# Performance work log

Measured on AMD Instinct MI355X. Metric: run time of the kernel, lower is better.

The kernel has to match this reference:

```python
import jax, jax.numpy as jnp
import numpy as np

B, T, H, NH = 2, 2048, 2048, 16
HD = H // NH
EPS = 1e-5

def gelu_tanh(x):
    c = jnp.sqrt(jnp.asarray(2.0 / jnp.pi, x.dtype))
    return 0.5 * x * (1.0 + jnp.tanh(c * (x + 0.044715 * x * x * x)))

def layer_norm(x, scale, shift):
    mean = jnp.mean(x, axis=-1, keepdims=True)
    var = jnp.mean((x - mean) ** 2, axis=-1, keepdims=True)  # unbiased=False
    return scale * ((x - mean) / jnp.sqrt(var + EPS)) + shift

def setup_inputs() -> dict:
    key = jax.random.key(0)
    ks = jax.random.split(key, 8)
    s = 0.02
    return {
        "x": jax.random.normal(ks[0], (B, T, H), dtype=jnp.float32),
        "wq": jax.random.normal(ks[1], (H, H), dtype=jnp.float32) * s,
        "wk": jax.random.normal(ks[2], (H, H), dtype=jnp.float32) * s,
        "wv": jax.random.normal(ks[3], (H, H), dtype=jnp.float32) * s,
        "wo": jax.random.normal(ks[4], (H, H), dtype=jnp.float32) * s,
        "ln1_scale": jnp.ones((H,), jnp.float32),
        "ln1_shift": jnp.zeros((H,), jnp.float32),
        "ln2_scale": jnp.ones((H,), jnp.float32),
        "ln2_shift": jnp.zeros((H,), jnp.float32),
        "w1": jax.random.normal(ks[5], (H, 4 * H), dtype=jnp.float32) * s,
        "b1": jnp.zeros((4 * H,), jnp.float32),
        "w2": jax.random.normal(ks[6], (4 * H, H), dtype=jnp.float32) * s,
        "b2": jnp.zeros((H,), jnp.float32),
    }

def reference(x, wq, wk, wv, wo, ln1_scale, ln1_shift, ln2_scale, ln2_shift, w1, b1, w2, b2):
    b, t, c = x.shape
    # --- attention sublayer (pre-norm, residual) ---
    h = layer_norm(x, ln1_scale, ln1_shift)
    q = (h @ wq).reshape(b, t, NH, HD).transpose(0, 2, 1, 3)  # [b,nh,t,hd]
    k = (h @ wk).reshape(b, t, NH, HD).transpose(0, 2, 1, 3)
    v = (h @ wv).reshape(b, t, NH, HD).transpose(0, 2, 1, 3)
    scores = jnp.einsum('bhqd,bhkd->bhqk', q, k) / jnp.sqrt(jnp.asarray(HD, jnp.float32))
    causal = jnp.triu(jnp.ones((t, t), jnp.bool_), k=1)
    scores = jnp.where(causal, -jnp.inf, scores)
    weights = jax.nn.softmax(scores, axis=-1)
    attn = jnp.einsum('bhqk,bhkd->bhqd', weights, v)
    attn = attn.transpose(0, 2, 1, 3).reshape(b, t, c)
    x = x + attn @ wo  # dropout is identity (drop_rate=0)
    # --- FFN sublayer ---
    h = layer_norm(x, ln2_scale, ln2_shift)
    h = gelu_tanh(h @ w1 + b1) @ w2 + b2
    return x + h
```

## Files before the change

kernel.cpp:

```cpp
#include <hip/hip_runtime.h>
#include <math.h>

#define HDIM 2048
#define NTOK 4096
#define NHEAD 16
#define HEADD 128
#define TSEQ 2048
#define NBATCH 2

typedef float f32x4 __attribute__((ext_vector_type(4)));
typedef short bf16x8 __attribute__((ext_vector_type(8)));

__device__ __forceinline__ unsigned short f2bf(float f) {
  union { float f; unsigned u; } v; v.f = f;
  unsigned r = v.u + 0x7FFFu + ((v.u >> 16) & 1u);
  return (unsigned short)(r >> 16);
}

__device__ __forceinline__ float gelu_tanh_f(float x) {
  float z = 0.7978845608028654f * (x + 0.044715f * x * x * x);
  float e = __expf(2.f * z);
  float th = 1.f - 2.f / (e + 1.f);
  return 0.5f * x * (1.f + th);
}

#define GLL16(g, l) __builtin_amdgcn_global_load_lds( \
    (const __attribute__((address_space(1))) unsigned int*)(g), \
    (__attribute__((address_space(3))) unsigned int*)(l), 16, 0, 0)

__global__ __launch_bounds__(256) void ln_kernel(const float* __restrict__ in,
                                                 const float* __restrict__ scale,
                                                 const float* __restrict__ shift,
                                                 unsigned short* __restrict__ out) {
  int row = blockIdx.x;
  int t = threadIdx.x;
  const float4* r4 = (const float4*)(in + (size_t)row * HDIM);
  float4 v0 = r4[t];
  float4 v1 = r4[t + 256];
  float sum = v0.x + v0.y + v0.z + v0.w + v1.x + v1.y + v1.z + v1.w;
  float sq  = v0.x*v0.x + v0.y*v0.y + v0.z*v0.z + v0.w*v0.w +
              v1.x*v1.x + v1.y*v1.y + v1.z*v1.z + v1.w*v1.w;
  for (int o = 32; o > 0; o >>= 1) {
    sum += __shfl_down(sum, o);
    sq  += __shfl_down(sq, o);
  }
  __shared__ float red[8];
  __shared__ float stat[2];
  int lane = t & 63, w = t >> 6;
  if (lane == 0) { red[w] = sum; red[4 + w] = sq; }
  __syncthreads();
  if (t == 0) {
    float s = red[0] + red[1] + red[2] + red[3];
    float q = red[4] + red[5] + red[6] + red[7];
    float mean = s / HDIM;
    float var = q / HDIM - mean * mean;
    stat[0] = mean;
    stat[1] = rsqrtf(var + 1e-5f);
  }
  __syncthreads();
  float mean = stat[0], rstd = stat[1];
  const float4* sc4 = (const float4*)scale;
  const float4* sh4 = (const float4*)shift;
  float4 s0 = sc4[t], s1 = sc4[t + 256];
  float4 h0 = sh4[t], h1 = sh4[t + 256];
  ushort4 a, b;
  a.x = f2bf(s0.x * ((v0.x - mean) * rstd) + h0.x);
  a.y = f2bf(s0.y * ((v0.y - mean) * rstd) + h0.y);
  a.z = f2bf(s0.z * ((v0.z - mean) * rstd) + h0.z);
  a.w = f2bf(s0.w * ((v0.w - mean) * rstd) + h0.w);
  b.x = f2bf(s1.x * ((v1.x - mean) * rstd) + h1.x);
  b.y = f2bf(s1.y * ((v1.y - mean) * rstd) + h1.y);
  b.z = f2bf(s1.z * ((v1.z - mean) * rstd) + h1.z);
  b.w = f2bf(s1.w * ((v1.w - mean) * rstd) + h1.w);
  *(ushort4*)&out[(size_t)row * HDIM + t * 4] = a;
  *(ushort4*)&out[(size_t)row * HDIM + 1024 + t * 4] = b;
}

__global__ __launch_bounds__(256) void castT_kernel(const float* __restrict__ W,
                                                    unsigned short* __restrict__ Wt,
                                                    int K, int N) {
  __shared__ float T[64][65];
  int k0 = blockIdx.x * 64, n0 = blockIdx.y * 64;
  int c = threadIdx.x & 15, r = threadIdx.x >> 4;
#pragma unroll
  for (int p = 0; p < 4; p++) {
    int kr = r + p * 16;
    float4 v = *(const float4*)&W[(size_t)(k0 + kr) * N + n0 + c * 4];
    T[kr][c * 4 + 0] = v.x; T[kr][c * 4 + 1] = v.y;
    T[kr][c * 4 + 2] = v.z; T[kr][c * 4 + 3] = v.w;
  }
  __syncthreads();
#pragma unroll
  for (int p = 0; p < 4; p++) {
    int nr = r + p * 16;
    ushort4 o;
    o.x = f2bf(T[c * 4 + 0][nr]);
    o.y = f2bf(T[c * 4 + 1][nr]);
    o.z = f2bf(T[c * 4 + 2][nr]);
    o.w = f2bf(T[c * 4 + 3][nr]);
    *(ushort4*)&Wt[(size_t)(n0 + nr) * K + k0 + c * 4] = o;
  }
}

template<int BN>
__global__ __launch_bounds__(512, 2) void gemm256(const unsigned short* __restrict__ A,
                                                  const unsigned short* __restrict__ Bt,
                                                  float* __restrict__ Cf,
                                                  unsigned short* __restrict__ Cb,
                                                  const float* __restrict__ bias,
                                                  const float* __restrict__ resid,
                                                  int M, int N, int K, int act_gelu,
                                                  int qkv_mode,
                                                  unsigned short* __restrict__ Qo,
                                                  unsigned short* __restrict__ Ko,
                                                  unsigned short* __restrict__ Vto,
                                                  int rm, int rn, int xc) {
  constexpr int NIT = BN / 64;
  constexpr int NB  = NIT / 2;
  constexpr int BSZ = BN * 64;

  __shared__ unsigned short ldsA[2 * 16384];
  __shared__ unsigned short ldsB[2 * BSZ];

  const int tid = threadIdx.x;
  const int w = tid >> 6, lane = tid & 63;
  const int lm = lane & 15, qd = lane >> 4;
  const int wm = w >> 2, wn = w & 3;
  const int l8 = lane >> 3, l7 = lane & 7;

  int flat = blockIdx.y * gridDim.x + blockIdx.x;
  int xcd = flat & 7, l = flat >> 3;
  int tn_l = l % rn, tm_l = l / rn;
  int tm = (xcd / xc) * rm + tm_l;
  int tn = (xcd % xc) * rn + tn_l;
  int m0 = tm * 256, n0 = tn * BN;

  const int swz = ((l7 ^ (l8 & 7)) << 3);
  const int arb = wm * 128 + (w & 3) * 16;
  const unsigned short* pAs = A + (size_t)(m0 + arb + l8) * K + swz;
  unsigned short* lAs = ldsA + arb * 64;
  const int brb = (BN == 256) ? ((w >> 1) * 64 + (w & 1) * 16)
                              : ((w >> 1) * 32 + (w & 1) * 8);
  const unsigned short* pBs = Bt + (size_t)(n0 + brb + l8) * K + swz;
  unsigned short* lBs = ldsB + brb * 64;

  const int ca0 = ((qd ^ l7) << 3);
  const unsigned short* pAr = ldsA + (wm * 128 + lm) * 64;
  const unsigned short* pBr = ldsB + (wn * (BN / 4) + lm) * 64;

  f32x4 acc[8][NIT] = {};
  bf16x8 a[2][4], b[2][NB];

#define STAGE_A(buf, qm, kt) do { \
    const unsigned short* _s = pAs + (size_t)(qm) * 64 * K + (size_t)(kt) * 64; \
    unsigned short* _d = lAs + (buf) * 16384 + (qm) * 4096; \
    GLL16(_s, _d); \
    GLL16(_s + (size_t)8 * K, _d + 512); \
  } while (0)

#define STAGE_B(buf, qn, kt) do { \
    if (BN == 256) { \
      const unsigned short* _s = pBs + (size_t)(qn) * 32 * K + (size_t)(kt) * 64; \
      unsigned short* _d = lBs + (buf) * BSZ + (qn) * 2048; \
      GLL16(_s, _d); \
      GLL16(_s + (size_t)8 * K, _d + 512); \
    } else { \
      const unsigned short* _s = pBs + (size_t)(qn) * 16 * K + (size_t)(kt) * 64; \
      unsigned short* _d = lBs + (buf) * BSZ + (qn) * 1024; \
      GLL16(_s, _d); \
    } \
  } while (0)

#define LDA(buf, qm) do { \
    _Pragma("unroll") \
    for (int mi = 0; mi < 4; mi++) { \
      a[0][mi] = *(const bf16x8*)(pAr + (buf) * 16384 + (qm) * 4096 + mi * 1024 + ca0); \
      a[1][mi] = *(const bf16x8*)(pAr + (buf) * 16384 + (qm) * 4096 + mi * 1024 + (ca0 ^ 32)); \
    } \
  } while (0)

#define LDB(buf, qn) do { \
    _Pragma("unroll") \
    for (int ni = 0; ni < NB; ni++) { \
      b[0][ni] = *(const bf16x8*)(pBr + (buf) * BSZ + (qn) * (NB * 1024) + ni * 1024 + ca0); \
      b[1][ni] = *(const bf16x8*)(pBr + (buf) * BSZ + (qn) * (NB * 1024) + ni * 1024 + (ca0 ^ 32)); \
    } \
  } while (0)

#define MFMA_PH(qm, qn) do { \
    __builtin_amdgcn_s_setprio(1); \
    _Pragma("unroll") \
    for (int ks = 0; ks < 2; ks++) \
      _Pragma("unroll") \
      for (int mi = 0; mi < 4; mi++) \
        _Pragma("unroll") \
        for (int ni = 0; ni < NB; ni++) \
          acc[(qm) * 4 + mi][(qn) * NB + ni] = __builtin_amdgcn_mfma_f32_16x16x32_bf16( \
              a[ks][mi], b[ks][ni], acc[(qm) * 4 + mi][(qn) * NB + ni], 0, 0, 0); \
    __builtin_amdgcn_s_setprio(0); \
  } while (0)

#define BARX() do { __builtin_amdgcn_sched_barrier(0); __builtin_amdgcn_s_barrier(); \
                    __builtin_amdgcn_sched_barrier(0); } while (0)
#define LGKM0() do { asm volatile("s_waitcnt lgkmcnt(0)"); \
                     __builtin_amdgcn_sched_barrier(0); } while (0)
#define VM_SS() do { if (BN == 256) asm volatile("s_waitcnt vmcnt(6)"); \
                     else           asm volatile("s_waitcnt vmcnt(5)"); \
                     __builtin_amdgcn_sched_barrier(0); } while (0)
#define VM_0()  do { asm volatile("s_waitcnt vmcnt(0)"); \
                     __builtin_amdgcn_sched_barrier(0); } while (0)

  const int niter = K >> 7;

  STAGE_A(0, 0, 0); STAGE_B(0, 1, 0); STAGE_A(0, 1, 0); STAGE_B(0, 0, 0);
  STAGE_A(1, 0, 1); STAGE_B(1, 1, 1); STAGE_A(1, 1, 1);
  VM_SS();
  BARX();

  for (int i = 0; i < niter; ++i) {
    const bool pf = (i + 1 < niter);
    const int te = 2 * i + 2, to = 2 * i + 3;
    LDA(0, 0); LDB(0, 0);
    STAGE_B(1, 0, 2 * i + 1);
    BARX(); LGKM0();
    MFMA_PH(0, 0);
    BARX();
    LDB(0, 1);
    if (pf) STAGE_A(0, 0, te);
    BARX(); LGKM0();
    MFMA_PH(0, 1);
    BARX();
    LDA(0, 1);
    if (pf) STAGE_B(0, 1, te);
    BARX(); LGKM0();
    MFMA_PH(1, 1);
    BARX();
    LDB(0, 0);
    if (pf) STAGE_A(0, 1, te);
    BARX(); LGKM0();
    MFMA_PH(1, 0);
    if (pf) VM_SS(); else VM_0();
    BARX();
    LDA(1, 0); LDB(1, 0);
    if (pf) STAGE_B(0, 0, te);
    BARX(); LGKM0();
    MFMA_PH(0, 0);
    BARX();
    LDB(1, 1);
    if (pf) STAGE_A(1, 0, to);
    BARX(); LGKM0();
    MFMA_PH(0, 1);
    BARX();
    LDA(1, 1);
    if (pf) STAGE_B(1, 1, to);
    BARX(); LGKM0();
    MFMA_PH(1, 1);
    BARX();
    LDB(1, 0);
    if (pf) STAGE_A(1, 1, to);
    BARX(); LGKM0();
    MFMA_PH(1, 0);
    if (pf) VM_SS();
    BARX();
  }

#undef STAGE_A
#undef STAGE_B
#undef LDA
#undef LDB
#undef MFMA_PH
#undef BARX
#undef LGKM0
#undef VM_SS
#undef VM_0

  if (qkv_mode) {
#pragma unroll
    for (int ni = 0; ni < NIT; ni++) {
      int n = n0 + wn * (BN / 4) + ni * 16 + lm;
      int region = n >> 11;
      int h = (n & 2047) >> 7, d = n & 127;
#pragma unroll
      for (int mi = 0; mi < 8; mi++) {
        int mb = m0 + wm * 128 + mi * 16 + qd * 4;
        int bb = mb >> 11, t0 = mb & 2047;
        if (region == 2) {
          ushort4 u;
          u.x = f2bf(acc[mi][ni][0]); u.y = f2bf(acc[mi][ni][1]);
          u.z = f2bf(acc[mi][ni][2]); u.w = f2bf(acc[mi][ni][3]);
          *(ushort4*)&Vto[(((size_t)(bb * NHEAD + h)) * HEADD + d) * TSEQ + t0] = u;
        } else {
          unsigned short* dst = (region == 0) ? Qo : Ko;
          size_t base2 = (((size_t)(bb * NHEAD + h)) * TSEQ + t0) * HEADD + d;
#pragma unroll
          for (int r = 0; r < 4; r++)
            dst[base2 + (size_t)r * HEADD] = f2bf(acc[mi][ni][r]);
        }
      }
    }
    return;
  }

#pragma unroll
  for (int ni = 0; ni < NIT; ni++) {
    int n = n0 + wn * (BN / 4) + ni * 16 + lm;
    float bv = bias ? bias[n] : 0.f;
#pragma unroll
    for (int mi = 0; mi < 8; mi++) {
#pragma unroll
      for (int r = 0; r < 4; r++) {
        int m = m0 + wm * 128 + mi * 16 + qd * 4 + r;
        float v = acc[mi][ni][r] + bv;
        if (act_gelu) v = gelu_tanh_f(v);
        if (resid) v += resid[(size_t)m * N + n];
        if (Cb) Cb[(size_t)m * N + n] = f2bf(v);
        else Cf[(size_t)m * N + n] = v;
      }
    }
  }
}

__global__ __launch_bounds__(256, 4) void attn_mfma(const unsigned short* __restrict__ Qb,
                                                    const unsigned short* __restrict__ Kb,
                                                    const unsigned short* __restrict__ Vtb,
                                                    unsigned short* __restrict__ O) {
  __shared__ unsigned short ldsK[64 * 128];
  __shared__ unsigned short ldsV[128 * 64];
  __shared__ unsigned short ldsP[64 * 64];

  int tid = threadIdx.x;
  int w = tid >> 6, lane = tid & 63;
  int lm = lane & 15, qd = lane >> 4;
  int qt = blockIdx.x, hh = blockIdx.y, bb = blockIdx.z;
  int q0 = qt * 64;
  size_t hbase = (size_t)(bb * NHEAD + hh) * (size_t)(TSEQ * HEADD);
  const unsigned short* Qh = Qb + hbase;
  const unsigned short* Kh = Kb + hbase;
  const unsigned short* Vh = Vtb + hbase;

  bf16x8 qf[4];
  {
    const unsigned short* qp = Qh + (size_t)(q0 + w * 16 + lm) * HEADD + qd * 8;
#pragma unroll
    for (int kc = 0; kc < 4; kc++) qf[kc] = *(const bf16x8*)(qp + kc * 32);
  }

  int koff[4], voff[4], ldst[4];
#pragma unroll
  for (int it = 0; it < 4; it++) {
    int ci = it * 256 + w * 64 + lane;
    int key = ci >> 4, pos = ci & 15;
    koff[it] = key * HEADD + ((pos ^ (key & 15)) << 3);
    int d = ci >> 3, pv = ci & 7;
    voff[it] = d * TSEQ + ((pv ^ (d & 7)) << 3);
    ldst[it] = (it * 256 + w * 64) * 8;
  }

  f32x4 oacc[8] = {};
  float mrow[4], lrow[4];
#pragma unroll
  for (int r = 0; r < 4; r++) { mrow[r] = -3.0e38f; lrow[r] = 0.f; }
  const float scl = 0.08838834764831845f;

  for (int kt = 0; kt <= qt; kt++) {
    int k0 = kt * 64;
    __syncthreads();
#pragma unroll
    for (int it = 0; it < 4; it++) {
      GLL16(Kh + (size_t)k0 * HEADD + koff[it], ldsK + ldst[it]);
      GLL16(Vh + k0 + voff[it], ldsV + ldst[it]);
    }
    __syncthreads();

    f32x4 sacc[4] = {};
#pragma unroll
    for (int kb = 0; kb < 4; kb++) {
#pragma unroll
      for (int kc = 0; kc < 4; kc++) {
        bf16x8 kf = *(const bf16x8*)(ldsK + (kb * 16 + lm) * HEADD + (((kc * 4 + qd) ^ lm) << 3));
        sacc[kb] = __builtin_amdgcn_mfma_f32_16x16x32_bf16(qf[kc], kf, sacc[kb], 0, 0, 0);
      }
    }

    float sv[4][4];
    int qrow_g = q0 + w * 16 + qd * 4;
    bool diag = (kt == qt);
#pragma unroll
    for (int kb = 0; kb < 4; kb++) {
      int key_g = k0 + kb * 16 + lm;
#pragma unroll
      for (int r = 0; r < 4; r++) {
        float x = sacc[kb][r] * scl;
        sv[kb][r] = (diag && key_g > qrow_g + r) ? -3.0e38f : x;
      }
    }
    float mloc[4];
#pragma unroll
    for (int r = 0; r < 4; r++)
      mloc[r] = fmaxf(fmaxf(sv[0][r], sv[1][r]), fmaxf(sv[2][r], sv[3][r]));
#pragma unroll
    for (int dm = 1; dm < 16; dm <<= 1)
#pragma unroll
      for (int r = 0; r < 4; r++) mloc[r] = fmaxf(mloc[r], __shfl_xor(mloc[r], dm));
    float al[4], lloc[4];
#pragma unroll
    for (int r = 0; r < 4; r++) {
      float mnew = fmaxf(mrow[r], mloc[r]);
      al[r] = __expf(mrow[r] - mnew);
      mrow[r] = mnew;
      lloc[r] = 0.f;
    }
#pragma unroll
    for (int kb = 0; kb < 4; kb++) {
#pragma unroll
      for (int r = 0; r < 4; r++) {
        float p = __expf(sv[kb][r] - mrow[r]);
        lloc[r] += p;
        int row = w * 16 + qd * 4 + r;
        int chunk = (kb * 2 + (lm >> 3)) ^ (row & 7);
        ldsP[row * 64 + chunk * 8 + (lm & 7)] = f2bf(p);
      }
    }
#pragma unroll
    for (int dm = 1; dm < 16; dm <<= 1)
#pragma unroll
      for (int r = 0; r < 4; r++) lloc[r] += __shfl_xor(lloc[r], dm);
#pragma unroll
    for (int r = 0; r < 4; r++) lrow[r] = lrow[r] * al[r] + lloc[r];
#pragma unroll
    for (int dt = 0; dt < 8; dt++)
#pragma unroll
      for (int r = 0; r < 4; r++) oacc[dt][r] *= al[r];

    bf16x8 pf[2];
#pragma unroll
    for (int kc2 = 0; kc2 < 2; kc2++)
      pf[kc2] = *(const bf16x8*)(ldsP + (w * 16 + lm) * 64 + (((kc2 * 4 + qd) ^ (lm & 7)) << 3));
#pragma unroll
    for (int dt = 0; dt < 8; dt++) {
#pragma unroll
      for (int kc2 = 0; kc2 < 2; kc2++) {
        bf16x8 vf = *(const bf16x8*)(ldsV + (dt * 16 + lm) * 64 + (((kc2 * 4 + qd) ^ (lm & 7)) << 3));
        oacc[dt] = __builtin_amdgcn_mfma_f32_16x16x32_bf16(pf[kc2], vf, oacc[dt], 0, 0, 0);
      }
    }
  }

  float inv[4];
#pragma unroll
  for (int r = 0; r < 4; r++) inv[r] = 1.f / lrow[r];
#pragma unroll
  for (int dt = 0; dt < 8; dt++) {
#pragma unroll
    for (int r = 0; r < 4; r++) {
      int t = q0 + w * 16 + qd * 4 + r;
      size_t idx = ((size_t)(bb * TSEQ + t)) * HDIM + hh * HEADD + dt * 16 + lm;
      O[idx] = f2bf(oacc[dt][r] * inv[r]);
    }
  }
}

extern "C" void kernel_launch(void* const* d_in, const int* in_sizes, int n_in,
                              void* d_out, int out_size, void* d_ws, size_t ws_size,
                              hipStream_t stream) {
  const float* x         = (const float*)d_in[0];
  const float* wq        = (const float*)d_in[1];
  const float* wk        = (const float*)d_in[2];
  const float* wv        = (const float*)d_in[3];
  const float* wo        = (const float*)d_in[4];
  const float* ln1_scale = (const float*)d_in[5];
  const float* ln1_shift = (const float*)d_in[6];
  const float* ln2_scale = (const float*)d_in[7];
  const float* ln2_shift = (const float*)d_in[8];
  const float* w1        = (const float*)d_in[9];
  const float* b1        = (const float*)d_in[10];
  const float* w2        = (const float*)d_in[11];
  const float* b2        = (const float*)d_in[12];

  char* ws = (char*)d_ws;
  const size_t MB = 1ull << 20;
  unsigned short* h1    = (unsigned short*)(ws);
  float*          x2    = (float*)(ws);
  unsigned short* Qb    = (unsigned short*)(ws + 32 * MB);
  unsigned short* Kb    = (unsigned short*)(ws + 48 * MB);
  unsigned short* Vtb   = (unsigned short*)(ws + 64 * MB);
  unsigned short* attnO = (unsigned short*)(ws + 80 * MB);
  unsigned short* woT   = (unsigned short*)(ws + 96 * MB);
  unsigned short* qkvT  = (unsigned short*)(ws + 104 * MB);
  unsigned short* a1    = (unsigned short*)(ws + 32 * MB);
  unsigned short* h2    = (unsigned short*)(ws + 96 * MB);
  unsigned short* w1T   = (unsigned short*)(ws + 128 * MB);
  unsigned short* w2T   = (unsigned short*)(ws + 160 * MB);

  dim3 blk(256), blk5(512);
  ln_kernel<<<NTOK, blk, 0, stream>>>(x, ln1_scale, ln1_shift, h1);
  castT_kernel<<<dim3(32, 32), blk, 0, stream>>>(wq, qkvT, 2048, 2048);
  castT_kernel<<<dim3(32, 32), blk, 0, stream>>>(wk, qkvT + (size_t)2048 * 2048, 2048, 2048);
  castT_kernel<<<dim3(32, 32), blk, 0, stream>>>(wv, qkvT + (size_t)4096 * 2048, 2048, 2048);
  castT_kernel<<<dim3(32, 32), blk, 0, stream>>>(wo, woT, 2048, 2048);
  castT_kernel<<<dim3(32, 128), blk, 0, stream>>>(w1, w1T, 2048, 8192);
  castT_kernel<<<dim3(128, 32), blk, 0, stream>>>(w2, w2T, 8192, 2048);
  gemm256<128><<<dim3(48, 16), blk5, 0, stream>>>(
      h1, qkvT, nullptr, nullptr, nullptr, nullptr, 4096, 6144, 2048, 0, 1, Qb, Kb, Vtb,
      8, 12, 4);
  attn_mfma<<<dim3(TSEQ / 64, NHEAD, NBATCH), blk, 0, stream>>>(Qb, Kb, Vtb, attnO);
  gemm256<128><<<dim3(16, 16), blk5, 0, stream>>>(
      attnO, woT, x2, nullptr, nullptr, x, 4096, 2048, 2048, 0, 0, nullptr, nullptr, nullptr,
      4, 8, 2);
  ln_kernel<<<NTOK, blk, 0, stream>>>(x2, ln2_scale, ln2_shift, h2);
  gemm256<256><<<dim3(32, 16), blk5, 0, stream>>>(
      h2, w1T, nullptr, a1, b1, nullptr, 4096, 8192, 2048, 1, 0, nullptr, nullptr, nullptr,
      8, 8, 4);
  gemm256<128><<<dim3(16, 16), blk5, 0, stream>>>(
      a1, w2T, (float*)d_out, nullptr, b2, x2, 4096, 2048, 8192, 0, 0, nullptr, nullptr, nullptr,
      4, 8, 2);
}
```

Before: 1.084 ms.

## Give BN=128 GEMM its own triple-buffered pipeline and 4x2 warp layout

The BN=128 variant of the GEMM gets a separate main loop: three LDS buffers with prefetch two K-tiles ahead, and a warp layout of 4x2 warps each owning a 64x64 subtile with a 4x4 MFMA accumulator, instead of 2x4 warps with 8x2 accumulators. The aim is to hide more global-load latency and to cut per-warp LDS traffic for this tile shape. The BN=256 path is unchanged. Triple buffering raises LDS use, which may lower occupancy for the BN=128 kernel.

Measured after the change: 975.6 us. -10.0%, faster.

```diff
diff --git a/kernel.cpp b/kernel.cpp
--- a/kernel.cpp
+++ b/kernel.cpp
@@ -115,17 +115,17 @@
                                                   unsigned short* __restrict__ Ko,
                                                   unsigned short* __restrict__ Vto,
                                                   int rm, int rn, int xc) {
-  constexpr int NIT = BN / 64;
-  constexpr int NB  = NIT / 2;
-  constexpr int BSZ = BN * 64;
-
-  __shared__ unsigned short ldsA[2 * 16384];
-  __shared__ unsigned short ldsB[2 * BSZ];
+  constexpr int BSZ  = BN * 64;
+  constexpr int AM   = (BN == 256) ? 8 : 4;
+  constexpr int AN   = 4;
+  constexpr int NBUF = (BN == 256) ? 2 : 3;
+
+  __shared__ unsigned short ldsA[NBUF * 16384];
+  __shared__ unsigned short ldsB[NBUF * BSZ];
 
   const int tid = threadIdx.x;
   const int w = tid >> 6, lane = tid & 63;
   const int lm = lane & 15, qd = lane >> 4;
-  const int wm = w >> 2, wn = w & 3;
   const int l8 = lane >> 3, l7 = lane & 7;
 
   int flat = blockIdx.y * gridDim.x + blockIdx.x;
@@ -136,7 +136,7 @@
   int m0 = tm * 256, n0 = tn * BN;
 
   const int swz = ((l7 ^ (l8 & 7)) << 3);
-  const int arb = wm * 128 + (w & 3) * 16;
+  const int arb = (w >> 2) * 128 + (w & 3) * 16;
   const unsigned short* pAs = A + (size_t)(m0 + arb + l8) * K + swz;
   unsigned short* lAs = ldsA + arb * 64;
   const int brb = (BN == 256) ? ((w >> 1) * 64 + (w & 1) * 16)
@@ -144,12 +144,23 @@
   const unsigned short* pBs = Bt + (size_t)(n0 + brb + l8) * K + swz;
   unsigned short* lBs = ldsB + brb * 64;
 
+  const int wrA = (BN == 256) ? (w >> 2) * 128 : (w >> 1) * 64;
+  const int wcB = (BN == 256) ? (w & 3) * 64  : (w & 1) * 64;
+
   const int ca0 = ((qd ^ l7) << 3);
-  const unsigned short* pAr = ldsA + (wm * 128 + lm) * 64;
-  const unsigned short* pBr = ldsB + (wn * (BN / 4) + lm) * 64;
-
-  f32x4 acc[8][NIT] = {};
-  bf16x8 a[2][4], b[2][NB];
+  const unsigned short* pAr = ldsA + (wrA + lm) * 64;
+  const unsigned short* pBr = ldsB + (wcB + lm) * 64;
+
+  f32x4 acc[AM][AN] = {};
+
+#define BARX() do { __builtin_amdgcn_sched_barrier(0); __builtin_amdgcn_s_barrier(); \
+                    __builtin_amdgcn_sched_barrier(0); } while (0)
+#define LGKM0() do { asm volatile("s_waitcnt lgkmcnt(0)"); \
+                     __builtin_amdgcn_sched_barrier(0); } while (0)
+#define VM6() do { asm volatile("s_waitcnt vmcnt(6)"); \
+                   __builtin_amdgcn_sched_barrier(0); } while (0)
+#define VM_0() do { asm volatile("s_waitcnt vmcnt(0)"); \
+                    __builtin_amdgcn_sched_barrier(0); } while (0)
 
 #define STAGE_A(buf, qm, kt) do { \
     const unsigned short* _s = pAs + (size_t)(qm) * 64 * K + (size_t)(kt) * 64; \
@@ -158,17 +169,15 @@
     GLL16(_s + (size_t)8 * K, _d + 512); \
   } while (0)
 
+  if constexpr (BN == 256) {
+    const int niter = K >> 7;
+    bf16x8 a[2][4], b[2][2];
+
 #define STAGE_B(buf, qn, kt) do { \
-    if (BN == 256) { \
-      const unsigned short* _s = pBs + (size_t)(qn) * 32 * K + (size_t)(kt) * 64; \
-      unsigned short* _d = lBs + (buf) * BSZ + (qn) * 2048; \
-      GLL16(_s, _d); \
-      GLL16(_s + (size_t)8 * K, _d + 512); \
-    } else { \
-      const unsigned short* _s = pBs + (size_t)(qn) * 16 * K + (size_t)(kt) * 64; \
-      unsigned short* _d = lBs + (buf) * BSZ + (qn) * 1024; \
-      GLL16(_s, _d); \
-    } \
+    const unsigned short* _s = pBs + (size_t)(qn) * 32 * K + (size_t)(kt) * 64; \
+    unsigned short* _d = lBs + (buf) * BSZ + (qn) * 2048; \
+    GLL16(_s, _d); \
+    GLL16(_s + (size_t)8 * K, _d + 512); \
   } while (0)
 
 #define LDA(buf, qm) do { \
@@ -181,9 +190,9 @@
 
 #define LDB(buf, qn) do { \
     _Pragma("unroll") \
-    for (int ni = 0; ni < NB; ni++) { \
-      b[0][ni] = *(const bf16x8*)(pBr + (buf) * BSZ + (qn) * (NB * 1024) + ni * 1024 + ca0); \
-      b[1][ni] = *(const bf16x8*)(pBr + (buf) * BSZ + (qn) * (NB * 1024) + ni * 1024 + (ca0 ^ 32)); \
+    for (int ni = 0; ni < 2; ni++) { \
+      b[0][ni] = *(const bf16x8*)(pBr + (buf) * BSZ + (qn) * 2048 + ni * 1024 + ca0); \
+      b[1][ni] = *(const bf16x8*)(pBr + (buf) * BSZ + (qn) * 2048 + ni * 1024 + (ca0 ^ 32)); \
     } \
   } while (0)
 
@@ -194,95 +203,145 @@
       _Pragma("unroll") \
       for (int mi = 0; mi < 4; mi++) \
         _Pragma("unroll") \
-        for (int ni = 0; ni < NB; ni++) \
-          acc[(qm) * 4 + mi][(qn) * NB + ni] = __builtin_amdgcn_mfma_f32_16x16x32_bf16( \
-              a[ks][mi], b[ks][ni], acc[(qm) * 4 + mi][(qn) * NB + ni], 0, 0, 0); \
+        for (int ni = 0; ni < 2; ni++) \
+          acc[(qm) * 4 + mi][(qn) * 2 + ni] = __builtin_amdgcn_mfma_f32_16x16x32_bf16( \
+              a[ks][mi], b[ks][ni], acc[(qm) * 4 + mi][(qn) * 2 + ni], 0, 0, 0); \
     __builtin_amdgcn_s_setprio(0); \
   } while (0)
 
-#define BARX() do { __builtin_amdgcn_sched_barrier(0); __builtin_amdgcn_s_barrier(); \
-                    __builtin_amdgcn_sched_barrier(0); } while (0)
-#define LGKM0() do { asm volatile("s_waitcnt lgkmcnt(0)"); \
-                     __builtin_amdgcn_sched_barrier(0); } while (0)
-#define VM_SS() do { if (BN == 256) asm volatile("s_waitcnt vmcnt(6)"); \
-                     else           asm volatile("s_waitcnt vmcnt(5)"); \
-                     __builtin_amdgcn_sched_barrier(0); } while (0)
-#define VM_0()  do { asm volatile("s_waitcnt vmcnt(0)"); \
-                     __builtin_amdgcn_sched_barrier(0); } while (0)
-
-  const int niter = K >> 7;
-
-  STAGE_A(0, 0, 0); STAGE_B(0, 1, 0); STAGE_A(0, 1, 0); STAGE_B(0, 0, 0);
-  STAGE_A(1, 0, 1); STAGE_B(1, 1, 1); STAGE_A(1, 1, 1);
-  VM_SS();
-  BARX();
-
-  for (int i = 0; i < niter; ++i) {
-    const bool pf = (i + 1 < niter);
-    const int te = 2 * i + 2, to = 2 * i + 3;
-    LDA(0, 0); LDB(0, 0);
-    STAGE_B(1, 0, 2 * i + 1);
-    BARX(); LGKM0();
-    MFMA_PH(0, 0);
+    STAGE_A(0, 0, 0); STAGE_B(0, 1, 0); STAGE_A(0, 1, 0); STAGE_B(0, 0, 0);
+    STAGE_A(1, 0, 1); STAGE_B(1, 1, 1); STAGE_A(1, 1, 1);
+    VM6();
     BARX();
-    LDB(0, 1);
-    if (pf) STAGE_A(0, 0, te);
-    BARX(); LGKM0();
-    MFMA_PH(0, 1);
-    BARX();
-    LDA(0, 1);
-    if (pf) STAGE_B(0, 1, te);
-    BARX(); LGKM0();
-    MFMA_PH(1, 1);
-    BARX();
-    LDB(0, 0);
-    if (pf) STAGE_A(0, 1, te);
-    BARX(); LGKM0();
-    MFMA_PH(1, 0);
-    if (pf) VM_SS(); else VM_0();
-    BARX();
-    LDA(1, 0); LDB(1, 0);
-    if (pf) STAGE_B(0, 0, te);
-    BARX(); LGKM0();
-    MFMA_PH(0, 0);
-    BARX();
-    LDB(1, 1);
-    if (pf) STAGE_A(1, 0, to);
-    BARX(); LGKM0();
-    MFMA_PH(0, 1);
-    BARX();
-    LDA(1, 1);
-    if (pf) STAGE_B(1, 1, to);
-    BARX(); LGKM0();
-    MFMA_PH(1, 1);
-    BARX();
-    LDB(1, 0);
-    if (pf) STAGE_A(1, 1, to);
-    BARX(); LGKM0();
-    MFMA_PH(1, 0);
-    if (pf) VM_SS();
-    BARX();
-  }
-
-#undef STAGE_A
+
+    for (int i = 0; i < niter; ++i) {
+      const bool pf = (i + 1 < niter);
+      const int te = 2 * i + 2, to = 2 * i + 3;
+      LDA(0, 0); LDB(0, 0);
+      STAGE_B(1, 0, 2 * i + 1);
+      BARX(); LGKM0();
+      MFMA_PH(0, 0);
+      BARX();
+      LDB(0, 1);
+      if (pf) STAGE_A(0, 0, te);
+      BARX(); LGKM0();
+      MFMA_PH(0, 1);
+      BARX();
+      LDA(0, 1);
+      if (pf) STAGE_B(0, 1, te);
+      BARX(); LGKM0();
+      MFMA_PH(1, 1);
+      BARX();
+      LDB(0, 0);
+      if (pf) STAGE_A(0, 1, te);
+      BARX(); LGKM0();
+      MFMA_PH(1, 0);
+      if (pf) VM6(); else VM_0();
+      BARX();
+      LDA(1, 0); LDB(1, 0);
+      if (pf) STAGE_B(0, 0, te);
+      BARX(); LGKM0();
+      MFMA_PH(0, 0);
+      BARX();
+      LDB(1, 1);
+      if (pf) STAGE_A(1, 0, to);
+      BARX(); LGKM0();
+      MFMA_PH(0, 1);
+      BARX();
+      LDA(1, 1);
+      if (pf) STAGE_B(1, 1, to);
+      BARX(); LGKM0();
+      MFMA_PH(1, 1);
+      BARX();
+      LDB(1, 0);
+      if (pf) STAGE_A(1, 1, to);
+      BARX(); LGKM0();
+      MFMA_PH(1, 0);
+      if (pf) VM6();
+      BARX();
+    }
 #undef STAGE_B
 #undef LDA
 #undef LDB
 #undef MFMA_PH
+
+  } else {
+    const int ntiles = K >> 6;
+    bf16x8 a2[4], b2[4];
+
+#define SB128(buf, kt) do { \
+    const unsigned short* _s = pBs + (size_t)(kt) * 64; \
+    unsigned short* _d = lBs + (buf) * BSZ; \
+    GLL16(_s, _d); \
+    GLL16(_s + (size_t)16 * K, _d + 1024); \
+  } while (0)
+
+#define LDA128(buf, ks) do { \
+    _Pragma("unroll") \
+    for (int mi = 0; mi < 4; mi++) \
+      a2[mi] = *(const bf16x8*)(pAr + (buf) * 16384 + mi * 1024 + ((ks) ? (ca0 ^ 32) : ca0)); \
+  } while (0)
+
+#define LDB128(buf, ks) do { \
+    _Pragma("unroll") \
+    for (int ni = 0; ni < 4; ni++) \
+      b2[ni] = *(const bf16x8*)(pBr + (buf) * BSZ + ni * 1024 + ((ks) ? (ca0 ^ 32) : ca0)); \
+  } while (0)
+
+#define MFMA16() do { \
+    __builtin_amdgcn_s_setprio(1); \
+    _Pragma("unroll") \
+    for (int mi = 0; mi < 4; mi++) \
+      _Pragma("unroll") \
+      for (int ni = 0; ni < 4; ni++) \
+        acc[mi][ni] = __builtin_amdgcn_mfma_f32_16x16x32_bf16( \
+            a2[mi], b2[ni], acc[mi][ni], 0, 0, 0); \
+    __builtin_amdgcn_s_setprio(0); \
+  } while (0)
+
+    STAGE_A(0, 0, 0); STAGE_A(0, 1, 0); SB128(0, 0);
+    STAGE_A(1, 0, 1); STAGE_A(1, 1, 1); SB128(1, 1);
+    VM6();
+    BARX();
+
+    int buf = 0, bs = 2;
+    for (int t = 0; t < ntiles; ++t) {
+      const bool pf = (t + 2 < ntiles);
+      LDA128(buf, 0); LDB128(buf, 0);
+      if (pf) { STAGE_A(bs, 0, t + 2); STAGE_A(bs, 1, t + 2); }
+      BARX(); LGKM0();
+      MFMA16();
+      BARX();
+      LDA128(buf, 1); LDB128(buf, 1);
+      if (pf) SB128(bs, t + 2);
+      BARX(); LGKM0();
+      MFMA16();
+      if (pf) VM6(); else if (t + 1 < ntiles) VM_0();
+      BARX();
+      buf = (buf == 2) ? 0 : buf + 1;
+      bs  = (bs  == 2) ? 0 : bs  + 1;
+    }
+#undef SB128
+#undef LDA128
+#undef LDB128
+#undef MFMA16
+  }
+
+#undef STAGE_A
 #undef BARX
 #undef LGKM0
-#undef VM_SS
+#undef VM6
 #undef VM_0
 
   if (qkv_mode) {
 #pragma unroll
-    for (int ni = 0; ni < NIT; ni++) {
-      int n = n0 + wn * (BN / 4) + ni * 16 + lm;
+    for (int ni = 0; ni < AN; ni++) {
+      int n = n0 + wcB + ni * 16 + lm;
       int region = n >> 11;
       int h = (n & 2047) >> 7, d = n & 127;
 #pragma unroll
-      for (int mi = 0; mi < 8; mi++) {
-        int mb = m0 + wm * 128 + mi * 16 + qd * 4;
+      for (int mi = 0; mi < AM; mi++) {
+        int mb = m0 + wrA + mi * 16 + qd * 4;
         int bb = mb >> 11, t0 = mb & 2047;
         if (region == 2) {
           ushort4 u;
@@ -302,14 +361,14 @@
   }
 
 #pragma unroll
-  for (int ni = 0; ni < NIT; ni++) {
-    int n = n0 + wn * (BN / 4) + ni * 16 + lm;
+  for (int ni = 0; ni < AN; ni++) {
+    int n = n0 + wcB + ni * 16 + lm;
     float bv = bias ? bias[n] : 0.f;
 #pragma unroll
-    for (int mi = 0; mi < 8; mi++) {
+    for (int mi = 0; mi < AM; mi++) {
 #pragma unroll
       for (int r = 0; r < 4; r++) {
-        int m = m0 + wm * 128 + mi * 16 + qd * 4 + r;
+        int m = m0 + wrA + mi * 16 + qd * 4 + r;
         float v = acc[mi][ni][r] + bv;
         if (act_gelu) v = gelu_tanh_f(v);
         if (resid) v += resid[(size_t)m * N + n];
```
